# Optimization experiments

Hardware: AMD Instinct MI355X
Metric: run time of the kernel (lower is better)

The kernel has to match this reference:

```python
import jax, jax.numpy as jnp
import numpy as np

B, NN, NC, H, V, K = 1024, 16, 16, 64, 100, 8
C = NN + NC
NEG = -1e9


def _ln_all(x, eps=1e-5):
    # torch.layer_norm(x, x.shape): normalize over ALL elements, no affine
    mu = x.mean()
    var = ((x - mu) ** 2).mean()
    return (x - mu) * jax.lax.rsqrt(var + eps)


def _ln_last(x, g, b, eps=1e-5):
    # nn.LayerNorm(H) with affine params
    mu = x.mean(-1, keepdims=True)
    var = ((x - mu) ** 2).mean(-1, keepdims=True)
    return (x - mu) * jax.lax.rsqrt(var + eps) * g + b


def _masked_ln(x, m, eps=1e-5):
    # x: [C,B,H], m: [C,B]; full-tensor layernorm over in-graph nodes only
    cnt = jnp.maximum(m.sum(1) * x.shape[-1], 1.0)
    mu = (x * m[..., None]).sum((1, 2)) / cnt
    d = x - mu[:, None, None]
    var = ((d * d) * m[..., None]).sum((1, 2)) / cnt
    return d * jax.lax.rsqrt(var + eps)[:, None, None]


def _forward(num_data, cat_data, num_w, num_b, cat_emb, fi_w1, fi_b1, fi_g, fi_be,
             fi_w2, fi_b2, gcn1_w, gcn1_b, gcn2_w, gcn2_b, pw1, pb1, pg, pbe, pw2, pb2):
    # numeric columns: Linear(1,H) per column == scalar * w + b
    fe_num = num_data[..., None] * num_w[None] + num_b[None]              # [B,NN,H]
    fe_num = _ln_all(jax.nn.relu(fe_num.reshape(B, NN * H)))
    fe_cat = cat_emb[jnp.arange(NC)[None, :], cat_data]                   # [B,NC,H]
    fe_cat = _ln_all(fe_cat.reshape(B, NC * H))
    feat = jnp.concatenate([fe_num, fe_cat], axis=1)                      # [B,C*H]
    fe3 = feat.reshape(B, C, H)
    # shared feature-importance MLP applied to every column slice (dropout = eval)
    h = _ln_last(jax.nn.relu(fe3 @ fi_w1 + fi_b1), fi_g, fi_be)
    imp = _ln_all((h @ fi_w2 + fi_b2)[..., 0])                            # [B,C]
    fe3 = fe3 * imp[..., None]
    feat = fe3.reshape(B, C * H)
    # top-K column selection per row + masked softmax
    _, idx = jax.lax.top_k(imp, K)                                        # [B,K]
    mask = jnp.zeros((B, C), jnp.float32).at[jnp.arange(B)[:, None], idx].set(1.0)
    p = jax.nn.softmax(jnp.where(mask > 0, imp, NEG), axis=1) * mask      # [B,C]
    # graph c: nodes = rows with column c in their top-K; zero column c,
    # adjacency = P P^T with zero diagonal, softmax over nonzero entries
    mT = mask.T                                                           # [C,B]
    pm = p[None, :, :] * mT[:, :, None] * (1.0 - jnp.eye(C))[:, None, :]  # [C,B,C]
    S = jnp.einsum('cik,cjk->cij', pm, pm)                                # [C,B,B]
    S = S * (1.0 - jnp.eye(B))
    pos = S > 0
    mx = jnp.max(jnp.where(pos, S, -jnp.inf), axis=(1, 2))
    mx = jnp.where(jnp.isfinite(mx), mx, 0.0)
    E = jnp.where(pos, jnp.exp(S - mx[:, None, None]), 0.0)
    Z = E.sum((1, 2))
    w = E / jnp.where(Z > 0, Z, 1.0)[:, None, None]
    # GCNConv normalization: add self-loops (weight 1) for in-graph nodes
    A = w + jnp.eye(B)[None] * mT[:, :, None]
    deg = A.sum(-1)
    dinv = jnp.where(deg > 0, jax.lax.rsqrt(deg), 0.0)
    An = dinv[:, :, None] * A * dinv[:, None, :]                          # [C,B,B]
    x = jnp.einsum('cij,jh->cih', An, feat @ gcn1_w) + gcn1_b
    x = _masked_ln(jax.nn.relu(x), mT)
    x = jnp.einsum('cij,cjh->cih', An, x @ gcn2_w) + gcn2_b
    x = _masked_ln(jax.nn.relu(x), mT)                                    # [C,B,H]
    # reassembly: each row gathers its K graph outputs, ordered by column id
    cols = jnp.sort(idx, axis=1)                                          # [B,K]
    gathered = x[cols, jnp.arange(B)[:, None]]                            # [B,K,H]
    full = jnp.concatenate([gathered, fe3], axis=1).reshape(B, (K + C) * H)
    return _ln_last(jax.nn.relu(full @ pw1 + pb1), pg, pbe) @ pw2 + pb2   # [B,2]


def setup_inputs() -> dict:
    key = jax.random.key(0)
    ks = jax.random.split(key, 12)
    s = 0.05
    f = jnp.float32
    return {
        'num_data': jax.random.normal(ks[0], (B, NN), f),
        'cat_data': jax.random.randint(ks[1], (B, NC), 0, V, jnp.int32),
        'num_w': jax.random.normal(ks[2], (NN, H), f) * s,
        'num_b': jnp.zeros((NN, H), f),
        'cat_emb': jax.random.normal(ks[3], (NC, V, H), f) * s,
        'fi_w1': jax.random.normal(ks[4], (H, H), f) * s,
        'fi_b1': jnp.zeros((H,), f),
        'fi_g': jnp.ones((H,), f),
        'fi_be': jnp.zeros((H,), f),
        'fi_w2': jax.random.normal(ks[5], (H, 1), f) * s,
        'fi_b2': jnp.zeros((1,), f),
        'gcn1_w': jax.random.normal(ks[6], (C * H, H), f) * s,
        'gcn1_b': jnp.zeros((H,), f),
        'gcn2_w': jax.random.normal(ks[7], (H, H), f) * s,
        'gcn2_b': jnp.zeros((H,), f),
        'pw1': jax.random.normal(ks[8], ((K + C) * H, H), f) * s,
        'pb1': jnp.zeros((H,), f),
        'pg': jnp.ones((H,), f),
        'pbe': jnp.zeros((H,), f),
        'pw2': jax.random.normal(ks[9], (H, 2), f) * s,
        'pb2': jnp.zeros((2,), f),
    }


def reference(num_data, cat_data, num_w, num_b, cat_emb, fi_w1, fi_b1, fi_g, fi_be,
              fi_w2, fi_b2, gcn1_w, gcn1_b, gcn2_w, gcn2_b, pw1, pb1, pg, pbe, pw2, pb2):
    return _forward(num_data, cat_data, num_w, num_b, cat_emb, fi_w1, fi_b1, fi_g, fi_be,
                    fi_w2, fi_b2, gcn1_w, gcn1_b, gcn2_w, gcn2_b, pw1, pb1, pg, pbe, pw2, pb2)
```

## Files before the change

kernel.cpp:

```cpp
#include <hip/hip_runtime.h>
#include <hip/hip_bf16.h>

#define BB   1024
#define NNUM 16
#define NCAT 16
#define HH   64
#define VV   100
#define KK   8
#define CC   32
#define CH   2048
#define FULLW 2560

#define OFF_FE3   0u
#define OFF_X1    2097152u
#define OFF_X2    4194304u
#define OFF_G     6291456u
#define OFF_SIMP  6356992u
#define OFF_P     6389760u
#define OFF_ROWE  6422528u
#define OFF_DINV  6455296u
#define OFF_F     6488064u
#define OFF_STATS 6520832u
#define OFF_Z     6520840u
#define OFF_X1S   6520872u
#define OFF_X2S   6520936u
#define OFF_COLS  6521000u
#define OFF_LIST  6529192u
#define OFF_CNT   6561960u
#define OFF_AOFF  6561992u
#define OFF_AN    6562048u

__device__ inline float wsum64(float v){
  #pragma unroll
  for (int o = 32; o; o >>= 1) v += __shfl_xor(v, o);
  return v;
}

__global__ __launch_bounds__(256) void k_init(float* ws){
  int t = threadIdx.x;
  if (t < 8)  ws[OFF_STATS + t] = 0.f;
  if (t < 64) ws[OFF_X1S + t] = 0.f;
  if (t < 64) ws[OFF_X2S + t] = 0.f;
  if (t < 32) ws[OFF_Z + t] = 0.f;
}

__global__ __launch_bounds__(256) void k_fe(const float* __restrict__ nd,
                                            const float* __restrict__ nw,
                                            const float* __restrict__ nb,
                                            const int* __restrict__ cd,
                                            const float* __restrict__ emb,
                                            float* __restrict__ ws){
  float* fe3 = ws + OFF_FE3;
  float lsn = 0.f, lssn = 0.f, lsc = 0.f, lssc = 0.f;
  for (int idx = blockIdx.x*256 + threadIdx.x; idx < 2*BB*NNUM*HH; idx += gridDim.x*256){
    if (idx < BB*NNUM*HH){
      int h = idx & 63, n = (idx >> 6) & 15, b = idx >> 10;
      float v = fmaxf(nd[b*NNUM + n]*nw[n*HH + h] + nb[n*HH + h], 0.f);
      fe3[b*CH + n*HH + h] = v;
      lsn += v; lssn += v*v;
    } else {
      int i2 = idx - BB*NNUM*HH;
      int h = i2 & 63, cc = (i2 >> 6) & 15, b = i2 >> 10;
      int j = cd[b*NCAT + cc];
      float v = emb[((size_t)cc*VV + j)*HH + h];
      fe3[b*CH + (NNUM + cc)*HH + h] = v;
      lsc += v; lssc += v*v;
    }
  }
  __shared__ float sh[16];
  lsn = wsum64(lsn); lssn = wsum64(lssn);
  lsc = wsum64(lsc); lssc = wsum64(lssc);
  int w = threadIdx.x >> 6;
  if ((threadIdx.x & 63) == 0){ sh[w] = lsn; sh[4+w] = lssn; sh[8+w] = lsc; sh[12+w] = lssc; }
  __syncthreads();
  if (threadIdx.x == 0){
    atomicAdd(ws + OFF_STATS + 0, sh[0]+sh[1]+sh[2]+sh[3]);
    atomicAdd(ws + OFF_STATS + 1, sh[4]+sh[5]+sh[6]+sh[7]);
    atomicAdd(ws + OFF_STATS + 2, sh[8]+sh[9]+sh[10]+sh[11]);
    atomicAdd(ws + OFF_STATS + 3, sh[12]+sh[13]+sh[14]+sh[15]);
  }
}

__global__ __launch_bounds__(256) void k_normfe(float* __restrict__ ws){
  const float Ninv = 1.f/1048576.f;
  int idx = blockIdx.x*256 + threadIdx.x;
  float* fe3 = ws + OFF_FE3;
  const float* st = ws + OFF_STATS;
  int r = idx & (CH-1); int c = r >> 6;
  float s, ssq;
  if (c < NNUM){ s = st[0]; ssq = st[1]; } else { s = st[2]; ssq = st[3]; }
  float mu = s*Ninv;
  float var = ssq*Ninv - mu*mu;
  float rs = rsqrtf(var + 1e-5f);
  fe3[idx] = (fe3[idx] - mu)*rs;
}

__global__ __launch_bounds__(256) void k_fi(const float* __restrict__ w1,
                                            const float* __restrict__ b1,
                                            const float* __restrict__ g,
                                            const float* __restrict__ be,
                                            const float* __restrict__ w2,
                                            const float* __restrict__ b2f,
                                            float* __restrict__ ws){
  __shared__ float w1s[64][65];
  __shared__ float xs[4][64];
  int wv = threadIdx.x >> 6, lane = threadIdx.x & 63;
  for (int q = threadIdx.x; q < 4096; q += 256) w1s[q >> 6][q & 63] = w1[q];
  __syncthreads();
  const float* fe3 = ws + OFF_FE3;
  float b1l = b1[lane], gl = g[lane], bel = be[lane], w2l = w2[lane], b2s = b2f[0];
  int gw = blockIdx.x*4 + wv;
  float ls = 0.f, lss = 0.f;
  for (int it = 0; it < 16; ++it){
    int row = gw + 2048*it;
    float x = fe3[(size_t)row*64 + lane];
    xs[wv][lane] = x;
    float t0 = 0.f, t1 = 0.f, t2 = 0.f, t3 = 0.f;
    #pragma unroll
    for (int k = 0; k < 64; k += 4){
      float4 xq = *(const float4*)&xs[wv][k];
      t0 += xq.x*w1s[k][lane];
      t1 += xq.y*w1s[k+1][lane];
      t2 += xq.z*w1s[k+2][lane];
      t3 += xq.w*w1s[k+3][lane];
    }
    float t = (t0+t1) + (t2+t3) + b1l;
    t = fmaxf(t, 0.f);
    float mu = wsum64(t)*(1.f/64.f);
    float d = t - mu;
    float var = wsum64(d*d)*(1.f/64.f);
    float rs = rsqrtf(var + 1e-5f);
    float h1 = d*rs*gl + bel;
    float s = wsum64(h1*w2l) + b2s;
    if (lane == 0) ws[OFF_SIMP + row] = s;
    ls += s; lss += s*s;
  }
  __shared__ float sh[8];
  if (lane == 0){ sh[wv] = ls; sh[4+wv] = lss; }
  __syncthreads();
  if (threadIdx.x == 0){
    atomicAdd(ws + OFF_STATS + 4, sh[0]+sh[1]+sh[2]+sh[3]);
    atomicAdd(ws + OFF_STATS + 5, sh[4]+sh[5]+sh[6]+sh[7]);
  }
}

__global__ __launch_bounds__(256) void k_topk(float* __restrict__ ws){
  int b = blockIdx.x;
  __shared__ float imp[CC];
  if (threadIdx.x < CC){
    const float Ninv = 1.f/32768.f;
    float s4 = ws[OFF_STATS+4], s5 = ws[OFF_STATS+5];
    float mu = s4*Ninv, var = s5*Ninv - mu*mu;
    float rs = rsqrtf(var + 1e-5f);
    imp[threadIdx.x] = (ws[OFF_SIMP + b*CC + threadIdx.x] - mu)*rs;
  }
  __syncthreads();
  if (threadIdx.x == 0){
    unsigned taken = 0;
    float m0 = 0.f;
    for (int t = 0; t < KK; t++){
      float best = -1e30f; int bi = 0;
      for (int c = 0; c < CC; c++){
        if (!((taken >> c) & 1u) && imp[c] > best){ best = imp[c]; bi = c; }
      }
      taken |= 1u << bi;
      if (t == 0) m0 = best;
    }
    float sum = 0.f;
    int* cols = (int*)(ws + OFF_COLS);
    int tn = 0;
    for (int c = 0; c < CC; c++){
      if ((taken >> c) & 1u){ cols[b*KK + tn] = c; tn++; sum += expf(imp[c] - m0); }
    }
    float inv = 1.f/sum;
    for (int c = 0; c < CC; c++){
      float pv = ((taken >> c) & 1u) ? expf(imp[c] - m0)*inv : 0.f;
      ws[OFF_P + b*CC + c] = pv;
    }
  }
  __syncthreads();
  float* fe3 = ws + OFF_FE3;
  for (int kq = threadIdx.x; kq < CH; kq += 256){
    fe3[b*CH + kq] *= imp[kq >> 6];
  }
}

__global__ __launch_bounds__(256) void k_lists(float* __restrict__ ws){
  int c = blockIdx.x;
  __shared__ int cnt_s;
  if (threadIdx.x == 0) cnt_s = 0;
  __syncthreads();
  int* list = (int*)(ws + OFF_LIST);
  for (int b = threadIdx.x; b < BB; b += 256){
    if (ws[OFF_P + b*CC + c] > 0.f){
      int slot = atomicAdd(&cnt_s, 1);
      list[c*BB + slot] = b;
    }
  }
  __syncthreads();
  if (threadIdx.x == 0) ((int*)(ws + OFF_CNT))[c] = cnt_s;
}

__global__ void k_offs(float* __restrict__ ws){
  if (threadIdx.x == 0){
    const int* cnt = (const int*)(ws + OFF_CNT);
    int* aoff = (int*)(ws + OFF_AOFF);
    int acc = 0;
    for (int c = 0; c < CC; c++){ aoff[c] = acc; acc += cnt[c]*cnt[c]; }
    aoff[CC] = acc;
  }
}

__global__ __launch_bounds__(256) void k_G(const float* __restrict__ w1g, float* __restrict__ ws){
  __shared__ float frow[4][CH];
  int wv = threadIdx.x >> 6, lane = threadIdx.x & 63;
  int b = blockIdx.x*4 + wv;
  const float* fe3 = ws + OFF_FE3;
  for (int q = 0; q < 32; q++) frow[wv][q*64 + lane] = fe3[b*CH + q*64 + lane];
  __syncthreads();
  float a0 = 0.f, a1 = 0.f, a2 = 0.f, a3 = 0.f;
  #pragma unroll 8
  for (int k = 0; k < CH; k += 4){
    float4 fq = *(const float4*)&frow[wv][k];
    a0 += fq.x*w1g[(k+0)*64 + lane];
    a1 += fq.y*w1g[(k+1)*64 + lane];
    a2 += fq.z*w1g[(k+2)*64 + lane];
    a3 += fq.w*w1g[(k+3)*64 + lane];
  }
  ws[OFF_G + b*64 + lane] = (a0+a1) + (a2+a3);
}

__global__ __launch_bounds__(256) void k_E(float* __restrict__ ws){
  int c = blockIdx.x;
  int n = ((const int*)(ws + OFF_CNT))[c];
  int r0 = blockIdx.y*32;
  if (r0 >= n) return;
  const int* list = (const int*)(ws + OFF_LIST) + c*BB;
  const float* p = ws + OFF_P;
  int base = ((const int*)(ws + OFF_AOFF))[c];
  float* An = ws + OFF_AN;
  __shared__ float pis[32][36];
  __shared__ float pT[32][72];
  int wv = threadIdx.x >> 6, lane = threadIdx.x & 63;
  for (int idx = threadIdx.x; idx < 1024; idx += 256){
    int r = idx >> 5, u = idx & 31;
    int ii = r0 + r;
    float v = 0.f;
    if (ii < n && u != c) v = p[list[ii]*CC + u];
    pis[r][u] = v;
  }
  float re[8] = {0.f,0.f,0.f,0.f,0.f,0.f,0.f,0.f};
  int rowBase = r0 + wv*8;
  for (int jt = 0; jt < n; jt += 64){
    __syncthreads();
    for (int idx = threadIdx.x; idx < 2048; idx += 256){
      int t = idx & 63, u = idx >> 6;
      int jj = jt + t;
      float v = 0.f;
      if (jj < n) v = p[list[jj]*CC + u];
      pT[u][t] = v;
    }
    __syncthreads();
    int jj = jt + lane;
    bool jok = (jj < n);
    #pragma unroll
    for (int r = 0; r < 8; r++){
      int row = rowBase + r;
      if (row < n){
        float4 pi0 = *(const float4*)&pis[wv*8 + r][0];
        float4 pi1 = *(const float4*)&pis[wv*8 + r][4];
        float4 pi2 = *(const float4*)&pis[wv*8 + r][8];
        float4 pi3 = *(const float4*)&pis[wv*8 + r][12];
        float4 pi4 = *(const float4*)&pis[wv*8 + r][16];
        float4 pi5 = *(const float4*)&pis[wv*8 + r][20];
        float4 pi6 = *(const float4*)&pis[wv*8 + r][24];
        float4 pi7 = *(const float4*)&pis[wv*8 + r][28];
        float s0 = pi0.x*pT[0][lane]  + pi1.x*pT[4][lane]  + pi2.x*pT[8][lane]  + pi3.x*pT[12][lane]
                 + pi4.x*pT[16][lane] + pi5.x*pT[20][lane] + pi6.x*pT[24][lane] + pi7.x*pT[28][lane];
        float s1 = pi0.y*pT[1][lane]  + pi1.y*pT[5][lane]  + pi2.y*pT[9][lane]  + pi3.y*pT[13][lane]
                 + pi4.y*pT[17][lane] + pi5.y*pT[21][lane] + pi6.y*pT[25][lane] + pi7.y*pT[29][lane];
        float s2 = pi0.z*pT[2][lane]  + pi1.z*pT[6][lane]  + pi2.z*pT[10][lane] + pi3.z*pT[14][lane]
                 + pi4.z*pT[18][lane] + pi5.z*pT[22][lane] + pi6.z*pT[26][lane] + pi7.z*pT[30][lane];
        float s3 = pi0.w*pT[3][lane]  + pi1.w*pT[7][lane]  + pi2.w*pT[11][lane] + pi3.w*pT[15][lane]
                 + pi4.w*pT[19][lane] + pi5.w*pT[23][lane] + pi6.w*pT[27][lane] + pi7.w*pT[31][lane];
        float S = (s0+s1) + (s2+s3);
        float Ev = 0.f;
        if (jok && jj != row && S > 0.f) Ev = __expf(S);
        if (jok) An[(size_t)base + (size_t)row*n + jj] = Ev;
        re[r] += Ev;
      }
    }
  }
  float zpart = 0.f;
  #pragma unroll
  for (int r = 0; r < 8; r++){
    float rsum = wsum64(re[r]);
    int row = rowBase + r;
    if (lane == 0 && row < n){
      ws[OFF_ROWE + c*BB + row] = rsum;
      zpart += rsum;
    }
  }
  __shared__ float sh[4];
  if (lane == 0) sh[wv] = zpart;
  __syncthreads();
  if (threadIdx.x == 0) atomicAdd(ws + OFF_Z + c, sh[0]+sh[1]+sh[2]+sh[3]);
}

__global__ __launch_bounds__(256) void k_scl(float* __restrict__ ws){
  int c = blockIdx.x;
  int n = ((const int*)(ws + OFF_CNT))[c];
  int ii = blockIdx.y*256 + threadIdx.x;
  if (ii >= n) return;
  float z = ws[OFF_Z + c];
  float zp = (z > 0.f) ? z : 1.f;
  float re = ws[OFF_ROWE + c*BB + ii];
  float di = rsqrtf(re/zp + 1.0f);
  ws[OFF_DINV + c*BB + ii] = di;
  ws[OFF_F    + c*BB + ii] = di*rsqrtf(zp);
}

__global__ __launch_bounds__(256) void k_agg(const float* __restrict__ src, int chanStride,
                                             const float* __restrict__ bias,
                                             float* __restrict__ outb,
                                             float* __restrict__ statsb,
                                             float* __restrict__ ws){
  int c = blockIdx.x;
  int n = ((const int*)(ws + OFF_CNT))[c];
  int wv = __builtin_amdgcn_readfirstlane(threadIdx.x >> 6);
  int lane = threadIdx.x & 63;
  int ii = blockIdx.y*4 + wv;
  bool active = (ii < n);
  float s = 0.f, ssq = 0.f;
  if (active){
    int base = ((const int*)(ws + OFF_AOFF))[c];
    const int* lst = (const int*)(ws + OFF_LIST) + c*BB;
    const float* Erow = ws + OFF_AN + (size_t)base + (size_t)ii*n;
    const float* f = ws + OFF_F + c*BB;
    const float* srcc = src + (size_t)c*(size_t)chanStride*64;
    float acc = 0.f;
    int j = 0;
    for (; j + 16 <= n; j += 16){
      #pragma unroll
      for (int t = 0; t < 16; t++){
        float ef = Erow[j+t]*f[j+t];
        int jg = lst[j+t];
        acc += ef * srcc[(size_t)jg*64 + lane];
      }
    }
    for (; j < n; j++){
      float ef = Erow[j]*f[j];
      int jg = lst[j];
      acc += ef * srcc[(size_t)jg*64 + lane];
    }
    int i = lst[ii];
    float di = ws[OFF_DINV + c*BB + ii];
    float srow = srcc[(size_t)i*64 + lane];
    float a = f[ii]*acc + di*di*srow + bias[lane];
    a = fmaxf(a, 0.f);
    outb[((size_t)c*BB + i)*64 + lane] = a;
    s = wsum64(a); ssq = wsum64(a*a);
  }
  __shared__ float shs[4], shq[4];
  if (lane == 0){ shs[wv] = active ? s : 0.f; shq[wv] = active ? ssq : 0.f; }
  __syncthreads();
  if (threadIdx.x == 0){
    float ts = shs[0]+shs[1]+shs[2]+shs[3];
    float tq = shq[0]+shq[1]+shq[2]+shq[3];
    if (tq != 0.f){
      atomicAdd(statsb + 2*c,     ts);
      atomicAdd(statsb + 2*c + 1, tq);
    }
  }
}

__global__ __launch_bounds__(256) void k_y(const float* __restrict__ w2g, float* __restrict__ ws){
  __shared__ float w2s[64][65];
  __shared__ float xs[4][64];
  int wv = threadIdx.x >> 6, lane = threadIdx.x & 63;
  for (int q = threadIdx.x; q < 4096; q += 256) w2s[q >> 6][q & 63] = w2g[q];
  __syncthreads();
  int c = blockIdx.x;
  int n = ((const int*)(ws + OFF_CNT))[c];
  const int* list = (const int*)(ws + OFF_LIST);
  float* x1 = ws + OFF_X1;
  float cntf = fmaxf((float)(n*64), 1.f);
  float mu = ws[OFF_X1S + 2*c]/cntf;
  float var = ws[OFF_X1S + 2*c + 1]/cntf - mu*mu;
  float rs = rsqrtf(var + 1e-5f);
  for (int ii = blockIdx.y*4 + wv; ii < n; ii += 64){
    int i = list[c*BB + ii];
    size_t bse = ((size_t)c*BB + i)*64;
    float xn = (x1[bse + lane] - mu)*rs;
    xs[wv][lane] = xn;
    float y0 = 0.f, y1 = 0.f, y2 = 0.f, y3 = 0.f;
    #pragma unroll
    for (int k = 0; k < 64; k += 4){
      float4 xq = *(const float4*)&xs[wv][k];
      y0 += xq.x*w2s[k][lane];
      y1 += xq.y*w2s[k+1][lane];
      y2 += xq.z*w2s[k+2][lane];
      y3 += xq.w*w2s[k+3][lane];
    }
    x1[bse + lane] = (y0+y1) + (y2+y3);
  }
}

__global__ __launch_bounds__(256) void k_final(const float* __restrict__ pw1,
                                               const float* __restrict__ pb1,
                                               const float* __restrict__ pg,
                                               const float* __restrict__ pbe,
                                               const float* __restrict__ pw2,
                                               const float* __restrict__ pb2,
                                               float* __restrict__ ws,
                                               float* __restrict__ out){
  __shared__ float fr[4][FULLW];
  int wv = threadIdx.x >> 6, lane = threadIdx.x & 63;
  int b = blockIdx.x*4 + wv;
  const int* cols = (const int*)(ws + OFF_COLS);
  const int* cnt  = (const int*)(ws + OFF_CNT);
  const float* x2 = ws + OFF_X2;
  const float* fe3 = ws + OFF_FE3;
  #pragma unroll
  for (int t = 0; t < KK; t++){
    int ct = cols[b*KK + t];
    float cf = fmaxf((float)(cnt[ct]*64), 1.f);
    float mu = ws[OFF_X2S + 2*ct]/cf;
    float var = ws[OFF_X2S + 2*ct + 1]/cf - mu*mu;
    float rs = rsqrtf(var + 1e-5f);
    fr[wv][t*64 + lane] = (x2[((size_t)ct*BB + b)*64 + lane] - mu)*rs;
  }
  #pragma unroll
  for (int q = 0; q < 32; q++) fr[wv][512 + q*64 + lane] = fe3[b*CH + q*64 + lane];
  __syncthreads();
  float a0 = 0.f, a1 = 0.f, a2 = 0.f, a3 = 0.f;
  #pragma unroll 8
  for (int k = 0; k < FULLW; k += 4){
    float4 fq = *(const float4*)&fr[wv][k];
    a0 += fq.x*pw1[(k+0)*64 + lane];
    a1 += fq.y*pw1[(k+1)*64 + lane];
    a2 += fq.z*pw1[(k+2)*64 + lane];
    a3 += fq.w*pw1[(k+3)*64 + lane];
  }
  float acc = (a0+a1) + (a2+a3) + pb1[lane];
  acc = fmaxf(acc, 0.f);
  float mu = wsum64(acc)*(1.f/64.f);
  float d = acc - mu;
  float var = wsum64(d*d)*(1.f/64.f);
  float rs = rsqrtf(var + 1e-5f);
  float zn = d*rs*pg[lane] + pbe[lane];
  float s0 = wsum64(zn*pw2[lane*2 + 0]);
  float s1 = wsum64(zn*pw2[lane*2 + 1]);
  if (lane == 0){
    out[b*2 + 0] = s0 + pb2[0];
    out[b*2 + 1] = s1 + pb2[1];
  }
}

extern "C" void kernel_launch(void* const* d_in, const int* in_sizes, int n_in,
                              void* d_out, int out_size, void* d_ws, size_t ws_size,
                              hipStream_t stream){
  (void)in_sizes; (void)n_in; (void)out_size; (void)ws_size;
  const float* num_data = (const float*)d_in[0];
  const int*   cat_data = (const int*)d_in[1];
  const float* num_w   = (const float*)d_in[2];
  const float* num_b   = (const float*)d_in[3];
  const float* cat_emb = (const float*)d_in[4];
  const float* fi_w1   = (const float*)d_in[5];
  const float* fi_b1   = (const float*)d_in[6];
  const float* fi_g    = (const float*)d_in[7];
  const float* fi_be   = (const float*)d_in[8];
  const float* fi_w2   = (const float*)d_in[9];
  const float* fi_b2   = (const float*)d_in[10];
  const float* gcn1_w  = (const float*)d_in[11];
  const float* gcn1_b  = (const float*)d_in[12];
  const float* gcn2_w  = (const float*)d_in[13];
  const float* gcn2_b  = (const float*)d_in[14];
  const float* pw1     = (const float*)d_in[15];
  const float* pb1     = (const float*)d_in[16];
  const float* pg      = (const float*)d_in[17];
  const float* pbe     = (const float*)d_in[18];
  const float* pw2     = (const float*)d_in[19];
  const float* pb2     = (const float*)d_in[20];
  float* ws  = (float*)d_ws;
  float* out = (float*)d_out;

  k_init<<<1, 256, 0, stream>>>(ws);
  k_fe<<<2048, 256, 0, stream>>>(num_data, num_w, num_b, cat_data, cat_emb, ws);
  k_normfe<<<8192, 256, 0, stream>>>(ws);
  k_fi<<<512, 256, 0, stream>>>(fi_w1, fi_b1, fi_g, fi_be, fi_w2, fi_b2, ws);
  k_topk<<<1024, 256, 0, stream>>>(ws);
  k_lists<<<32, 256, 0, stream>>>(ws);
  k_offs<<<1, 64, 0, stream>>>(ws);
  k_G<<<256, 256, 0, stream>>>(gcn1_w, ws);
  k_E<<<dim3(32, 32), 256, 0, stream>>>(ws);
  k_scl<<<dim3(32, 4), 256, 0, stream>>>(ws);
  k_agg<<<dim3(32, 256), 256, 0, stream>>>(ws + OFF_G, 0, gcn1_b, ws + OFF_X1, ws + OFF_X1S, ws);
  k_y<<<dim3(32, 16), 256, 0, stream>>>(gcn2_w, ws);
  k_agg<<<dim3(32, 256), 256, 0, stream>>>(ws + OFF_X1, BB, gcn2_b, ws + OFF_X2, ws + OFF_X2S, ws);
  k_final<<<256, 256, 0, stream>>>(pw1, pb1, pg, pbe, pw2, pb2, ws, out);
}
```

Before: 633.0 us.

## Vectorize feature embed/normalize, widen FI grid, and batch GCN aggregation via shuffles

```diff
diff --git a/kernel.cpp b/kernel.cpp
--- a/kernel.cpp
+++ b/kernel.cpp
@@ -52,19 +52,28 @@
                                             float* __restrict__ ws){
   float* fe3 = ws + OFF_FE3;
   float lsn = 0.f, lssn = 0.f, lsc = 0.f, lssc = 0.f;
-  for (int idx = blockIdx.x*256 + threadIdx.x; idx < 2*BB*NNUM*HH; idx += gridDim.x*256){
-    if (idx < BB*NNUM*HH){
-      int h = idx & 63, n = (idx >> 6) & 15, b = idx >> 10;
-      float v = fmaxf(nd[b*NNUM + n]*nw[n*HH + h] + nb[n*HH + h], 0.f);
-      fe3[b*CH + n*HH + h] = v;
-      lsn += v; lssn += v*v;
+  int idx = blockIdx.x*256 + threadIdx.x;
+  {
+    int h4 = idx & 15, fn = (idx >> 4) & 15, b = (idx >> 8) & 1023;
+    bool isNum = (idx < 262144);
+    if (isNum){
+      float s = nd[b*NNUM + fn];
+      float4 w = *(const float4*)&nw[fn*HH + h4*4];
+      float4 bi = *(const float4*)&nb[fn*HH + h4*4];
+      float4 v;
+      v.x = fmaxf(s*w.x + bi.x, 0.f);
+      v.y = fmaxf(s*w.y + bi.y, 0.f);
+      v.z = fmaxf(s*w.z + bi.z, 0.f);
+      v.w = fmaxf(s*w.w + bi.w, 0.f);
+      *(float4*)&fe3[b*CH + fn*HH + h4*4] = v;
+      lsn = v.x+v.y+v.z+v.w;
+      lssn = v.x*v.x+v.y*v.y+v.z*v.z+v.w*v.w;
     } else {
-      int i2 = idx - BB*NNUM*HH;
-      int h = i2 & 63, cc = (i2 >> 6) & 15, b = i2 >> 10;
-      int j = cd[b*NCAT + cc];
-      float v = emb[((size_t)cc*VV + j)*HH + h];
-      fe3[b*CH + (NNUM + cc)*HH + h] = v;
-      lsc += v; lssc += v*v;
+      int j = cd[b*NCAT + fn];
+      float4 v = *(const float4*)&emb[((size_t)fn*VV + j)*HH + h4*4];
+      *(float4*)&fe3[b*CH + (NNUM + fn)*HH + h4*4] = v;
+      lsc = v.x+v.y+v.z+v.w;
+      lssc = v.x*v.x+v.y*v.y+v.z*v.z+v.w*v.w;
     }
   }
   __shared__ float sh[16];
@@ -74,25 +83,30 @@
   if ((threadIdx.x & 63) == 0){ sh[w] = lsn; sh[4+w] = lssn; sh[8+w] = lsc; sh[12+w] = lssc; }
   __syncthreads();
   if (threadIdx.x == 0){
-    atomicAdd(ws + OFF_STATS + 0, sh[0]+sh[1]+sh[2]+sh[3]);
-    atomicAdd(ws + OFF_STATS + 1, sh[4]+sh[5]+sh[6]+sh[7]);
-    atomicAdd(ws + OFF_STATS + 2, sh[8]+sh[9]+sh[10]+sh[11]);
-    atomicAdd(ws + OFF_STATS + 3, sh[12]+sh[13]+sh[14]+sh[15]);
+    if (blockIdx.x < 1024){
+      atomicAdd(ws + OFF_STATS + 0, sh[0]+sh[1]+sh[2]+sh[3]);
+      atomicAdd(ws + OFF_STATS + 1, sh[4]+sh[5]+sh[6]+sh[7]);
+    } else {
+      atomicAdd(ws + OFF_STATS + 2, sh[8]+sh[9]+sh[10]+sh[11]);
+      atomicAdd(ws + OFF_STATS + 3, sh[12]+sh[13]+sh[14]+sh[15]);
+    }
   }
 }
 
 __global__ __launch_bounds__(256) void k_normfe(float* __restrict__ ws){
   const float Ninv = 1.f/1048576.f;
-  int idx = blockIdx.x*256 + threadIdx.x;
+  int idx4 = blockIdx.x*256 + threadIdx.x;
   float* fe3 = ws + OFF_FE3;
   const float* st = ws + OFF_STATS;
-  int r = idx & (CH-1); int c = r >> 6;
+  int c = (idx4 & 511) >> 4;
   float s, ssq;
   if (c < NNUM){ s = st[0]; ssq = st[1]; } else { s = st[2]; ssq = st[3]; }
   float mu = s*Ninv;
   float var = ssq*Ninv - mu*mu;
   float rs = rsqrtf(var + 1e-5f);
-  fe3[idx] = (fe3[idx] - mu)*rs;
+  float4 v = *(float4*)&fe3[idx4*4];
+  v.x = (v.x - mu)*rs; v.y = (v.y - mu)*rs; v.z = (v.z - mu)*rs; v.w = (v.w - mu)*rs;
+  *(float4*)&fe3[idx4*4] = v;
 }
 
 __global__ __launch_bounds__(256) void k_fi(const float* __restrict__ w1,
@@ -111,8 +125,8 @@
   float b1l = b1[lane], gl = g[lane], bel = be[lane], w2l = w2[lane], b2s = b2f[0];
   int gw = blockIdx.x*4 + wv;
   float ls = 0.f, lss = 0.f;
-  for (int it = 0; it < 16; ++it){
-    int row = gw + 2048*it;
+  for (int it = 0; it < 8; ++it){
+    int row = gw + 4096*it;
     float x = fe3[(size_t)row*64 + lane];
     xs[wv][lane] = x;
     float t0 = 0.f, t1 = 0.f, t2 = 0.f, t3 = 0.f;
@@ -327,7 +341,7 @@
                                              float* __restrict__ ws){
   int c = blockIdx.x;
   int n = ((const int*)(ws + OFF_CNT))[c];
-  int wv = __builtin_amdgcn_readfirstlane(threadIdx.x >> 6);
+  int wv = threadIdx.x >> 6;
   int lane = threadIdx.x & 63;
   int ii = blockIdx.y*4 + wv;
   bool active = (ii < n);
@@ -338,25 +352,25 @@
     const float* Erow = ws + OFF_AN + (size_t)base + (size_t)ii*n;
     const float* f = ws + OFF_F + c*BB;
     const float* srcc = src + (size_t)c*(size_t)chanStride*64;
-    float acc = 0.f;
-    int j = 0;
-    for (; j + 16 <= n; j += 16){
-      #pragma unroll
-      for (int t = 0; t < 16; t++){
-        float ef = Erow[j+t]*f[j+t];
-        int jg = lst[j+t];
-        acc += ef * srcc[(size_t)jg*64 + lane];
+    float acc0 = 0.f, acc1 = 0.f;
+    for (int jb = 0; jb < n; jb += 64){
+      int jl = jb + lane;
+      float Ef = 0.f; int jg = 0;
+      if (jl < n){ Ef = Erow[jl]*f[jl]; jg = lst[jl]; }
+      #pragma unroll 8
+      for (int t = 0; t < 64; t += 2){
+        float ef0 = __shfl(Ef, t);
+        float ef1 = __shfl(Ef, t+1);
+        int jg0 = __shfl(jg, t);
+        int jg1 = __shfl(jg, t+1);
+        if (ef0 != 0.f) acc0 += ef0 * srcc[(size_t)jg0*64 + lane];
+        if (ef1 != 0.f) acc1 += ef1 * srcc[(size_t)jg1*64 + lane];
       }
-    }
-    for (; j < n; j++){
-      float ef = Erow[j]*f[j];
-      int jg = lst[j];
-      acc += ef * srcc[(size_t)jg*64 + lane];
     }
     int i = lst[ii];
     float di = ws[OFF_DINV + c*BB + ii];
     float srow = srcc[(size_t)i*64 + lane];
-    float a = f[ii]*acc + di*di*srow + bias[lane];
+    float a = f[ii]*(acc0 + acc1) + di*di*srow + bias[lane];
     a = fmaxf(a, 0.f);
     outb[((size_t)c*BB + i)*64 + lane] = a;
     s = wsum64(a); ssq = wsum64(a*a);
@@ -487,8 +501,8 @@
 
   k_init<<<1, 256, 0, stream>>>(ws);
   k_fe<<<2048, 256, 0, stream>>>(num_data, num_w, num_b, cat_data, cat_emb, ws);
-  k_normfe<<<8192, 256, 0, stream>>>(ws);
-  k_fi<<<512, 256, 0, stream>>>(fi_w1, fi_b1, fi_g, fi_be, fi_w2, fi_b2, ws);
+  k_normfe<<<2048, 256, 0, stream>>>(ws);
+  k_fi<<<1024, 256, 0, stream>>>(fi_w1, fi_b1, fi_g, fi_be, fi_w2, fi_b2, ws);
   k_topk<<<1024, 256, 0, stream>>>(ws);
   k_lists<<<32, 256, 0, stream>>>(ws);
   k_offs<<<1, 64, 0, stream>>>(ws);
```

New measurement: 1.007 ms. +59.0%, slower.
